# Kernel optimization log

Measured on AMD Instinct MI355X. Metric: run time of the kernel, lower is better.

The kernel has to match this reference:

```python
import jax, jax.numpy as jnp
import numpy as np

E, CIN, COUT, K = 8, 256, 256, 3
STRIDE, PAD, DIL, GROUPS = 1, 1, 1, 1
N, H, W = 32, 56, 56


def setup_inputs() -> dict:
    key = jax.random.key(0)
    k1, k2, k3 = jax.random.split(key, 3)
    x = jax.random.normal(k1, (N, CIN, H, W), jnp.float32)
    # expert weight bank: (E*COUT, CIN//GROUPS, K, K), as in the torch module
    weight = jax.random.normal(k2, (E * COUT, CIN // GROUPS, K, K), jnp.float32) * 0.05
    fc_w = jax.random.normal(k3, (E, CIN), jnp.float32) * 0.02
    fc_b = jnp.zeros((E,), jnp.float32)
    return {"x": x, "weight": weight, "fc_w": fc_w, "fc_b": fc_b}


def reference(x, weight, fc_w, fc_b):
    n = x.shape[0]
    # sigmoid gate from global-avg-pooled features: (n, E)
    gate = jax.nn.sigmoid(x.mean((2, 3)) @ fc_w.T + fc_b)
    # mix expert weights per sample: (n, COUT, CIN//GROUPS, K, K)
    w = (gate @ weight.reshape(E, -1)).reshape(n, COUT, CIN // GROUPS, K, K)

    def conv1(xi, wi):
        # xi: (CIN, H, W), wi: (COUT, CIN//GROUPS, K, K)
        return jax.lax.conv_general_dilated(
            xi[None], wi,
            window_strides=(STRIDE, STRIDE),
            padding=[(PAD, PAD), (PAD, PAD)],
            rhs_dilation=(DIL, DIL),
            feature_group_count=GROUPS,
            dimension_numbers=("NCHW", "OIHW", "NCHW"),
        )[0]

    return jax.vmap(conv1)(x, w)  # (n, COUT, H_out, W_out)
```

## Files before the change

kernel.cpp:

```cpp
#include <hip/hip_runtime.h>
#include <hip/hip_bf16.h>

#define E_    8
#define CIN_  256
#define COUT_ 256
#define NK    9
#define KTOT  2304
#define IMGH  56
#define IMGW  56
#define HW    3136
#define NBATCH 32
#define PADW  58
#define PADHW 3364

typedef __attribute__((ext_vector_type(8))) __bf16 bf16x8;
typedef __attribute__((ext_vector_type(4))) float f32x4;
typedef unsigned int u32;

__device__ __forceinline__ void gld_lds16(const __bf16* g, __bf16* l) {
    __builtin_amdgcn_global_load_lds(
        (const __attribute__((address_space(1))) void*)(g),
        (__attribute__((address_space(3))) void*)(l), 16, 0, 0);
}

__global__ __launch_bounds__(256) void init_kernel(__bf16* xTp, float* pooled) {
    const int tid0 = blockIdx.x * 256 + threadIdx.x;
    if (tid0 < NBATCH * CIN_) pooled[tid0] = 0.f;
    const int total = NBATCH * 228 * 128;
    u32* p = (u32*)xTp;
    for (int idx = tid0; idx < total; idx += gridDim.x * 256) {
        const int n  = idx / (228 * 128);
        const int r  = idx - n * (228 * 128);
        const int hp = r >> 7;
        const int cp = r & 127;
        int px;
        if (hp < 58)       px = hp;
        else if (hp < 116) px = 57 * PADW + (hp - 58);
        else if (hp < 172) px = (hp - 116 + 1) * PADW;
        else               px = (hp - 172 + 1) * PADW + 57;
        p[((size_t)(n * PADHW + px)) * 128 + cp] = 0u;
    }
}

__global__ __launch_bounds__(256) void transpose_kernel(const float* __restrict__ x,
                                                        __bf16* __restrict__ xTp,
                                                        float* __restrict__ pooled) {
    __shared__ __bf16 t[64][66];
    const int px0 = blockIdx.x * 64;
    const int c0  = blockIdx.y * 64;
    const int n   = blockIdx.z;
    const int tid = threadIdx.x;
    {
        const int px_l = tid & 63;
        const int cb   = (tid >> 6) * 16;
        #pragma unroll
        for (int i = 0; i < 16; ++i) {
            const int cin_l = cb + i;
            t[cin_l][px_l] =
                (__bf16)x[((size_t)(n * CIN_ + c0 + cin_l)) * HW + px0 + px_l];
        }
    }
    __syncthreads();
    {
        const int cin_l = tid & 63;
        const int pb    = (tid >> 6) * 16;
        float s = 0.f;
        #pragma unroll
        for (int i = 0; i < 16; ++i) {
            const int px = px0 + pb + i;
            const int h  = px / IMGW;
            const int w  = px - h * IMGW;
            const __bf16 v = t[cin_l][pb + i];
            s += (float)v;
            xTp[((size_t)(n * PADHW + (h + 1) * PADW + (w + 1))) * CIN_ + c0 + cin_l] = v;
        }
        atomicAdd(&pooled[n * CIN_ + c0 + cin_l], s);
    }
}

__global__ __launch_bounds__(256) void gate_kernel(const float* __restrict__ pooled,
                                                   const float* __restrict__ fc_w,
                                                   const float* __restrict__ fc_b,
                                                   float* __restrict__ gate) {
    const int t = threadIdx.x;
    const int n = t >> 3, e = t & 7;
    const float* pv = pooled + n * CIN_;
    const float* wv = fc_w + e * CIN_;
    float s = 0.f;
    for (int c = 0; c < CIN_; ++c) s += pv[c] * wv[c];
    s = s * (1.0f / HW) + fc_b[e];
    gate[t] = 1.0f / (1.0f + expf(-s));
}

__global__ __launch_bounds__(256) void mix_kernel(const float* __restrict__ weight,
                                                  const float* __restrict__ gate,
                                                  __bf16* __restrict__ wmix) {
    __shared__ float wstage[KTOT];
    __shared__ __bf16 tlds[KTOT];
    const int cout = blockIdx.x;
    const int n0   = blockIdx.y * 8;
    const int tid  = threadIdx.x;
    float wreg[E_][NK];
    for (int e = 0; e < E_; ++e) {
        const float* wp = weight + (size_t)(e * COUT_ + cout) * KTOT;
        #pragma unroll
        for (int i = 0; i < NK; ++i) wstage[tid + i * 256] = wp[tid + i * 256];
        __syncthreads();
        #pragma unroll
        for (int kk = 0; kk < NK; ++kk) wreg[e][kk] = wstage[tid * NK + kk];
        __syncthreads();
    }
    for (int n = n0; n < n0 + 8; ++n) {
        float g[E_];
        #pragma unroll
        for (int e = 0; e < E_; ++e) g[e] = gate[n * E_ + e];
        float acc[NK];
        #pragma unroll
        for (int kk = 0; kk < NK; ++kk) acc[kk] = 0.f;
        #pragma unroll
        for (int e = 0; e < E_; ++e)
            #pragma unroll
            for (int kk = 0; kk < NK; ++kk) acc[kk] += g[e] * wreg[e][kk];
        #pragma unroll
        for (int kk = 0; kk < NK; ++kk) tlds[kk * 256 + tid] = (__bf16)acc[kk];
        __syncthreads();
        u32* dst = (u32*)(wmix + ((size_t)(n * COUT_ + cout)) * KTOT);
        const u32* src = (const u32*)tlds;
        #pragma unroll
        for (int j = 0; j < 4; ++j) dst[tid + j * 256] = src[tid + j * 256];
        if (tid < 128) dst[tid + 1024] = src[tid + 1024];
        __syncthreads();
    }
}

#define BM 256
#define BN 224

__global__ __launch_bounds__(512) void conv_kernel(const __bf16* __restrict__ xTp,
                                                   const __bf16* __restrict__ wmix,
                                                   float* __restrict__ out) {
    __shared__ __attribute__((aligned(16))) __bf16 At[2][BM * 64];
    __shared__ __attribute__((aligned(16))) __bf16 Bt[2][BN * 64];

    const int bid = blockIdx.x;
    const int swz = (bid & 7) * 56 + (bid >> 3);
    const int n   = swz / 14;
    const int pt  = swz - n * 14;
    const int p0  = pt * BN;

    const int tid  = threadIdx.x;
    const int lane = tid & 63;
    const int wave = tid >> 6;
    const int lr   = lane >> 3;
    const int sl   = lane & 7;
    const int swzsl = sl ^ lr;

    const __bf16* wmixn = wmix + (size_t)n * COUT_ * KTOT;
    const __bf16* xTpn  = xTp + (size_t)n * PADHW * CIN_;

    const __bf16* asrc[4];
    #pragma unroll
    for (int i = 0; i < 4; ++i) {
        const int j = wave + 8 * i;
        asrc[i] = wmixn + (size_t)(8 * j + lr) * KTOT + swzsl * 8;
    }
    const __bf16* bsrc[4];
    int bj[4];
    #pragma unroll
    for (int i = 0; i < 4; ++i) {
        int j = wave + 8 * i; if (j > 27) j = 27;
        bj[i] = j;
        const int px = p0 + 8 * j + lr;
        const int h  = px / IMGW;
        const int w  = px - h * IMGW;
        bsrc[i] = xTpn + (size_t)(h * PADW + w) * CIN_ + swzsl * 8;
    }

    const f32x4 zero = {0.f, 0.f, 0.f, 0.f};
    f32x4 acc[4][7];
    #pragma unroll
    for (int i = 0; i < 4; ++i)
        #pragma unroll
        for (int j = 0; j < 7; ++j) acc[i][j] = zero;

    const int mbase = (wave >> 1) * 64;
    const int nbase = (wave & 1) * 112;
    const int fr = lane & 15;
    const int kg = lane >> 4;
    const int fswz = fr & 7;

    auto STAGE = [&](int buf, int step) {
        const int khw  = step >> 2;
        const int kh   = (khw * 11) >> 5;
        const int kw   = khw - kh * 3;
        const int aoff = step * 64;
        const int boff = (kh * PADW + kw) * 256 + (step & 3) * 64;
        #pragma unroll
        for (int i = 0; i < 4; ++i)
            gld_lds16(asrc[i] + aoff, &At[buf][(wave + 8 * i) * 512]);
        #pragma unroll
        for (int i = 0; i < 4; ++i)
            gld_lds16(bsrc[i] + boff, &Bt[buf][bj[i] * 512]);
    };

    auto COMPUTE = [&](const __bf16* Ab, const __bf16* Bb) {
        #pragma unroll
        for (int ks = 0; ks < 2; ++ks) {
            const int soff = ((ks * 4 + kg) ^ fswz) * 8;
            bf16x8 a[4], b[7];
            #pragma unroll
            for (int m = 0; m < 4; ++m)
                a[m] = *(const bf16x8*)(Ab + (mbase + m * 16 + fr) * 64 + soff);
            #pragma unroll
            for (int nn = 0; nn < 7; ++nn)
                b[nn] = *(const bf16x8*)(Bb + (nbase + nn * 16 + fr) * 64 + soff);
            #pragma unroll
            for (int m = 0; m < 4; ++m)
                #pragma unroll
                for (int nn = 0; nn < 7; ++nn)
                    acc[m][nn] = __builtin_amdgcn_mfma_f32_16x16x32_bf16(
                        a[m], b[nn], acc[m][nn], 0, 0, 0);
        }
    };

    STAGE(0, 0);
    for (int t = 0; t < 35; ++t) {
        const int buf = t & 1;
        STAGE(buf ^ 1, t + 1);
        asm volatile("s_waitcnt vmcnt(8)" ::: "memory");
        __builtin_amdgcn_s_barrier();
        COMPUTE(&At[buf][0], &Bt[buf][0]);
        __builtin_amdgcn_s_barrier();
    }
    asm volatile("s_waitcnt vmcnt(0)" ::: "memory");
    __builtin_amdgcn_s_barrier();
    COMPUTE(&At[1][0], &Bt[1][0]);

    const int rbase = kg * 4;
    #pragma unroll
    for (int m = 0; m < 4; ++m)
        #pragma unroll
        for (int nn = 0; nn < 7; ++nn) {
            float* op = out + (size_t)(n * COUT_ + mbase + m * 16 + rbase) * HW
                            + p0 + nbase + nn * 16 + fr;
            #pragma unroll
            for (int r = 0; r < 4; ++r)
                op[(size_t)r * HW] = acc[m][nn][r];
        }
}

extern "C" void kernel_launch(void* const* d_in, const int* in_sizes, int n_in,
                              void* d_out, int out_size, void* d_ws, size_t ws_size,
                              hipStream_t stream) {
    const float* x      = (const float*)d_in[0];
    const float* weight = (const float*)d_in[1];
    const float* fc_w   = (const float*)d_in[2];
    const float* fc_b   = (const float*)d_in[3];
    float* out = (float*)d_out;

    char* ws = (char*)d_ws;
    float* pooled = (float*)ws;
    float* gate   = (float*)(ws + 32 * 1024);
    __bf16* wmix  = (__bf16*)(ws + 64 * 1024);
    __bf16* xTp   = (__bf16*)(ws + 64 * 1024 +
                              (size_t)NBATCH * COUT_ * KTOT * 2);

    init_kernel<<<dim3(512), 256, 0, stream>>>(xTp, pooled);
    transpose_kernel<<<dim3(49, 4, NBATCH), 256, 0, stream>>>(x, xTp, pooled);
    gate_kernel<<<dim3(1), 256, 0, stream>>>(pooled, fc_w, fc_b, gate);
    mix_kernel<<<dim3(COUT_, 4), 256, 0, stream>>>(weight, gate, wmix);
    conv_kernel<<<dim3(448), 512, 0, stream>>>(xTp, wmix, out);
}
```

Measured before the change: 194.6 us.

## Use 256x256 conv tiles with 4-phase interleaved staging and MFMA scheduling

Raises the pixel tile from 224 to 256 (13 tiles per image, 416 blocks, last tile clamped and masked). Each wave now computes a 128x64 sub-tile, and the global-to-LDS loads for the next step are split into four quarter-stages interleaved with four MFMA phases. The phases are wrapped in barriers and s_setprio. The aim is to overlap memory with compute and raise MFMA density per LDS read. The cost is wasted work in the padded final tile and extra barriers per step.

```diff
diff --git a/kernel.cpp b/kernel.cpp
--- a/kernel.cpp
+++ b/kernel.cpp
@@ -134,7 +134,7 @@
 }
 
 #define BM 256
-#define BN 224
+#define BN 256
 
 __global__ __launch_bounds__(512) void conv_kernel(const __bf16* __restrict__ xTp,
                                                    const __bf16* __restrict__ wmix,
@@ -143,110 +143,151 @@
     __shared__ __attribute__((aligned(16))) __bf16 Bt[2][BN * 64];
 
     const int bid = blockIdx.x;
-    const int swz = (bid & 7) * 56 + (bid >> 3);
-    const int n   = swz / 14;
-    const int pt  = swz - n * 14;
+    const int swz = (bid & 7) * 52 + (bid >> 3);
+    const int n   = swz / 13;
+    const int pt  = swz - n * 13;
     const int p0  = pt * BN;
 
     const int tid  = threadIdx.x;
     const int lane = tid & 63;
     const int wave = tid >> 6;
-    const int lr   = lane >> 3;
-    const int sl   = lane & 7;
-    const int swzsl = sl ^ lr;
+    const int wr   = wave >> 2;
+    const int wc   = wave & 3;
+    const int fr   = lane & 15;
+    const int kg   = lane >> 4;
+    const int fswz = fr & 7;
 
     const __bf16* wmixn = wmix + (size_t)n * COUT_ * KTOT;
     const __bf16* xTpn  = xTp + (size_t)n * PADHW * CIN_;
 
-    const __bf16* asrc[4];
+    const int lr6 = tid >> 3;
+    const int ssl = (tid & 7) ^ (lr6 & 7);
+    const __bf16* aptr[4];
     #pragma unroll
     for (int i = 0; i < 4; ++i) {
-        const int j = wave + 8 * i;
-        asrc[i] = wmixn + (size_t)(8 * j + lr) * KTOT + swzsl * 8;
-    }
-    const __bf16* bsrc[4];
-    int bj[4];
+        const int g = ((i & 1) << 1) | (i >> 1);
+        aptr[i] = wmixn + (size_t)(g * 64 + lr6) * KTOT + ssl * 8;
+    }
+    const __bf16* bptr[4];
     #pragma unroll
-    for (int i = 0; i < 4; ++i) {
-        int j = wave + 8 * i; if (j > 27) j = 27;
-        bj[i] = j;
-        const int px = p0 + 8 * j + lr;
-        const int h  = px / IMGW;
-        const int w  = px - h * IMGW;
-        bsrc[i] = xTpn + (size_t)(h * PADW + w) * CIN_ + swzsl * 8;
+    for (int j = 0; j < 4; ++j) {
+        const int lds_row = j * 64 + lr6;
+        const int b32 = lds_row >> 5;
+        const int s   = ((b32 & 3) << 1) | (b32 >> 2);
+        int px = p0 + s * 32 + (lds_row & 31);
+        if (px > HW - 1) px = HW - 1;
+        const int h = px / IMGW;
+        const int w = px - h * IMGW;
+        bptr[j] = xTpn + (size_t)(h * PADW + w) * CIN_ + ssl * 8;
     }
 
     const f32x4 zero = {0.f, 0.f, 0.f, 0.f};
-    f32x4 acc[4][7];
+    f32x4 acc[8][4];
     #pragma unroll
-    for (int i = 0; i < 4; ++i)
-        #pragma unroll
-        for (int j = 0; j < 7; ++j) acc[i][j] = zero;
-
-    const int mbase = (wave >> 1) * 64;
-    const int nbase = (wave & 1) * 112;
-    const int fr = lane & 15;
-    const int kg = lane >> 4;
-    const int fswz = fr & 7;
-
-    auto STAGE = [&](int buf, int step) {
-        const int khw  = step >> 2;
-        const int kh   = (khw * 11) >> 5;
-        const int kw   = khw - kh * 3;
+    for (int i = 0; i < 8; ++i)
+        #pragma unroll
+        for (int j = 0; j < 4; ++j) acc[i][j] = zero;
+
+    const int so0 = (kg ^ fswz) * 8;
+    const int so1 = ((4 + kg) ^ fswz) * 8;
+    const int arow0 = wr * 64 + fr;
+    const int brow0 = wc * 32 + fr;
+
+    auto STAGE_A = [&](int buf, int step, int half) {
         const int aoff = step * 64;
+        gld_lds16(aptr[2 * half]     + aoff, &At[buf][(2 * half)     * 4096 + tid * 8]);
+        gld_lds16(aptr[2 * half + 1] + aoff, &At[buf][(2 * half + 1) * 4096 + tid * 8]);
+    };
+    auto STAGE_B = [&](int buf, int step, int half) {
+        const int khw = step >> 2;
+        const int kh  = (khw * 11) >> 5;
+        const int kw  = khw - kh * 3;
         const int boff = (kh * PADW + kw) * 256 + (step & 3) * 64;
-        #pragma unroll
-        for (int i = 0; i < 4; ++i)
-            gld_lds16(asrc[i] + aoff, &At[buf][(wave + 8 * i) * 512]);
-        #pragma unroll
-        for (int i = 0; i < 4; ++i)
-            gld_lds16(bsrc[i] + boff, &Bt[buf][bj[i] * 512]);
+        gld_lds16(bptr[2 * half]     + boff, &Bt[buf][(2 * half)     * 4096 + tid * 8]);
+        gld_lds16(bptr[2 * half + 1] + boff, &Bt[buf][(2 * half + 1) * 4096 + tid * 8]);
     };
 
-    auto COMPUTE = [&](const __bf16* Ab, const __bf16* Bb) {
-        #pragma unroll
-        for (int ks = 0; ks < 2; ++ks) {
-            const int soff = ((ks * 4 + kg) ^ fswz) * 8;
-            bf16x8 a[4], b[7];
-            #pragma unroll
-            for (int m = 0; m < 4; ++m)
-                a[m] = *(const bf16x8*)(Ab + (mbase + m * 16 + fr) * 64 + soff);
-            #pragma unroll
-            for (int nn = 0; nn < 7; ++nn)
-                b[nn] = *(const bf16x8*)(Bb + (nbase + nn * 16 + fr) * 64 + soff);
-            #pragma unroll
-            for (int m = 0; m < 4; ++m)
-                #pragma unroll
-                for (int nn = 0; nn < 7; ++nn)
-                    acc[m][nn] = __builtin_amdgcn_mfma_f32_16x16x32_bf16(
-                        a[m], b[nn], acc[m][nn], 0, 0, 0);
+    STAGE_A(0, 0, 0); STAGE_B(0, 0, 0); STAGE_B(0, 0, 1); STAGE_A(0, 0, 1);
+    asm volatile("s_waitcnt vmcnt(0)" ::: "memory");
+    __builtin_amdgcn_s_barrier();
+
+    bf16x8 a[4][2], b[4][2];
+
+    #define PH_BAR_IN  __builtin_amdgcn_s_barrier(); __builtin_amdgcn_s_setprio(1);
+    #define PH_BAR_OUT __builtin_amdgcn_s_setprio(0); __builtin_amdgcn_s_barrier();
+    #define MFMA_Q(mb, jb)                                                        \
+        _Pragma("unroll")                                                         \
+        for (int m = 0; m < 4; ++m)                                               \
+            _Pragma("unroll")                                                     \
+            for (int j = 0; j < 2; ++j) {                                         \
+                acc[mb + m][jb + j] = __builtin_amdgcn_mfma_f32_16x16x32_bf16(    \
+                    a[m][0], b[jb + j][0], acc[mb + m][jb + j], 0, 0, 0);         \
+                acc[mb + m][jb + j] = __builtin_amdgcn_mfma_f32_16x16x32_bf16(    \
+                    a[m][1], b[jb + j][1], acc[mb + m][jb + j], 0, 0, 0);         \
+            }
+    #define READ_A(mhalf)                                                         \
+        _Pragma("unroll")                                                         \
+        for (int m = 0; m < 4; ++m) {                                             \
+            const int ar = (mhalf) * 128 + arow0 + 16 * m;                        \
+            a[m][0] = *(const bf16x8*)(Ab + ar * 64 + so0);                       \
+            a[m][1] = *(const bf16x8*)(Ab + ar * 64 + so1);                       \
         }
-    };
-
-    STAGE(0, 0);
+    #define READ_B(jb)                                                            \
+        _Pragma("unroll")                                                         \
+        for (int j = 0; j < 2; ++j) {                                             \
+            const int br = ((jb + j) >> 1) * 128 + brow0 + ((jb + j) & 1) * 16;   \
+            b[jb + j][0] = *(const bf16x8*)(Bb + br * 64 + so0);                  \
+            b[jb + j][1] = *(const bf16x8*)(Bb + br * 64 + so1);                  \
+        }
+    #define VM6 asm volatile("s_waitcnt vmcnt(6)" ::: "memory");
+
     for (int t = 0; t < 35; ++t) {
         const int buf = t & 1;
-        STAGE(buf ^ 1, t + 1);
-        asm volatile("s_waitcnt vmcnt(8)" ::: "memory");
-        __builtin_amdgcn_s_barrier();
-        COMPUTE(&At[buf][0], &Bt[buf][0]);
-        __builtin_amdgcn_s_barrier();
-    }
-    asm volatile("s_waitcnt vmcnt(0)" ::: "memory");
-    __builtin_amdgcn_s_barrier();
-    COMPUTE(&At[1][0], &Bt[1][0]);
+        const int sb  = buf ^ 1;
+        const __bf16* Ab = &At[buf][0];
+        const __bf16* Bb = &Bt[buf][0];
+        STAGE_A(sb, t + 1, 0);
+        VM6;
+        READ_A(0); READ_B(0);
+        PH_BAR_IN;  MFMA_Q(0, 0); PH_BAR_OUT;
+        STAGE_B(sb, t + 1, 0);
+        VM6;
+        READ_B(2);
+        PH_BAR_IN;  MFMA_Q(0, 2); PH_BAR_OUT;
+        STAGE_B(sb, t + 1, 1);
+        VM6;
+        READ_A(1);
+        PH_BAR_IN;  MFMA_Q(4, 0); PH_BAR_OUT;
+        STAGE_A(sb, t + 1, 1);
+        VM6;
+        PH_BAR_IN;  MFMA_Q(4, 2); PH_BAR_OUT;
+    }
+    {
+        const __bf16* Ab = &At[1][0];
+        const __bf16* Bb = &Bt[1][0];
+        asm volatile("s_waitcnt vmcnt(0)" ::: "memory");
+        READ_A(0); READ_B(0);
+        PH_BAR_IN;  MFMA_Q(0, 0); PH_BAR_OUT;
+        READ_B(2);
+        PH_BAR_IN;  MFMA_Q(0, 2); PH_BAR_OUT;
+        READ_A(1);
+        PH_BAR_IN;  MFMA_Q(4, 0); PH_BAR_OUT;
+        PH_BAR_IN;  MFMA_Q(4, 2); PH_BAR_OUT;
+    }
 
     const int rbase = kg * 4;
-    #pragma unroll
-    for (int m = 0; m < 4; ++m)
-        #pragma unroll
-        for (int nn = 0; nn < 7; ++nn) {
-            float* op = out + (size_t)(n * COUT_ + mbase + m * 16 + rbase) * HW
-                            + p0 + nbase + nn * 16 + fr;
+    if (p0 + 64 * wc < HW) {
+        #pragma unroll
+        for (int m = 0; m < 8; ++m)
             #pragma unroll
-            for (int r = 0; r < 4; ++r)
-                op[(size_t)r * HW] = acc[m][nn][r];
-        }
+            for (int j = 0; j < 4; ++j) {
+                float* op = out + (size_t)(n * COUT_ + 128 * wr + m * 16 + rbase) * HW
+                                + p0 + 64 * wc + j * 16 + fr;
+                #pragma unroll
+                for (int r = 0; r < 4; ++r)
+                    op[(size_t)r * HW] = acc[m][j][r];
+            }
+    }
 }
 
 extern "C" void kernel_launch(void* const* d_in, const int* in_sizes, int n_in,
@@ -269,5 +310,5 @@
     transpose_kernel<<<dim3(49, 4, NBATCH), 256, 0, stream>>>(x, xTp, pooled);
     gate_kernel<<<dim3(1), 256, 0, stream>>>(pooled, fc_w, fc_b, gate);
     mix_kernel<<<dim3(COUT_, 4), 256, 0, stream>>>(weight, gate, wmix);
-    conv_kernel<<<dim3(448), 512, 0, stream>>>(xTp, wmix, out);
-}
+    conv_kernel<<<dim3(416), 512, 0, stream>>>(xTp, wmix, out);
+}
```

After: 211.4 us. 1.09x slower.
